# Optimization experiments

Measured on AMD Instinct MI355X. Metric: run time of the kernel, lower is better.

## Reference

```python
import jax, jax.numpy as jnp
import numpy as np

NUM_HEADS = 4
GROUPS = 8
EPS = 1e-5


def group_norm(x, w, b):
    B, C, H, W = x.shape
    xg = x.reshape(B, GROUPS, C // GROUPS, H, W)
    mu = jnp.mean(xg, axis=(2, 3, 4), keepdims=True)
    var = jnp.var(xg, axis=(2, 3, 4), keepdims=True)
    xg = (xg - mu) * jax.lax.rsqrt(var + EPS)
    x = xg.reshape(B, C, H, W)
    return x * w[None, :, None, None] + b[None, :, None, None]


def setup_inputs() -> dict:
    key = jax.random.key(0)
    k1, k2, k3 = jax.random.split(key, 3)
    B, C, H, W = 16, 256, 32, 32
    x = jax.random.normal(k1, (B, C, H, W), dtype=jnp.float32)
    gn_w = jnp.ones((C,), dtype=jnp.float32)
    gn_b = jnp.zeros((C,), dtype=jnp.float32)
    qkv_w = jax.random.normal(k2, (3 * C, C), dtype=jnp.float32) * 0.02
    qkv_b = jnp.zeros((3 * C,), dtype=jnp.float32)
    proj_w = jax.random.normal(k3, (C, C), dtype=jnp.float32) * 0.02
    proj_b = jnp.zeros((C,), dtype=jnp.float32)
    return {"x": x, "gn_w": gn_w, "gn_b": gn_b, "qkv_w": qkv_w,
            "qkv_b": qkv_b, "proj_w": proj_w, "proj_b": proj_b}


def reference(x, gn_w, gn_b, qkv_w, qkv_b, proj_w, proj_b):
    B, C, H, W = x.shape
    Dh = C // NUM_HEADS
    N = H * W
    skip = x
    xn = group_norm(x, gn_w, gn_b)
    # 1x1 conv QKV projection: [B,3C,H,W]
    qkv = jnp.einsum('oc,bchw->bohw', qkv_w, xn) + qkv_b[None, :, None, None]
    # split channel dim 3C -> [3, heads, Dh], flatten spatial -> N
    qkv = qkv.reshape(B, 3, NUM_HEADS, Dh, N)
    qkv = jnp.transpose(qkv, (1, 0, 2, 4, 3))  # [3,B,heads,N,Dh]
    q, k, v = qkv[0], qkv[1], qkv[2]
    scale = 1.0 / np.sqrt(Dh).astype(np.float32)
    attn = jnp.einsum('bhnd,bhmd->bhnm', q, k) * scale  # [B,heads,N,N]
    attn = jax.nn.softmax(attn, axis=-1)
    out = jnp.einsum('bhnm,bhmd->bhnd', attn, v)  # [B,heads,N,Dh]
    out = jnp.transpose(out, (0, 1, 3, 2)).reshape(B, C, H, W)
    out = jnp.einsum('oc,bchw->bohw', proj_w, out) + proj_b[None, :, None, None]
    return out + skip
```

## Files before the change

### kernel.cpp

```cpp
#include <hip/hip_runtime.h>

typedef unsigned short u16;
typedef __bf16 bf16x8 __attribute__((ext_vector_type(8)));
typedef float f32x4 __attribute__((ext_vector_type(4)));

#define QSCALE 0.18033688011112042f

__device__ __forceinline__ u16 f2bf(float f) {
  __bf16 h = (__bf16)f;
  union { __bf16 b; u16 u; } cv;
  cv.b = h;
  return cv.u;
}
__device__ __forceinline__ unsigned pack2(float a, float b) {
  return (unsigned)f2bf(a) | ((unsigned)f2bf(b) << 16);
}

__global__ __launch_bounds__(256) void prep(
    const float* __restrict__ qw, const float* __restrict__ pw,
    const float* __restrict__ x,
    u16* __restrict__ qwb, u16* __restrict__ pwb, float* __restrict__ stats) {
  __shared__ float sh1[256], sh2[256];
  const int blk = blockIdx.x;
  const int t = threadIdx.x;
  if (blk < 256) {
    int i = blk * 256 + t;
    const float* s; u16* d; int j;
    if (i < 49152) { s = qw; d = qwb; j = i; }
    else           { s = pw; d = pwb; j = i - 49152; }
    float4 v = *(const float4*)(s + (size_t)j * 4);
    uint2 o; o.x = pack2(v.x, v.y); o.y = pack2(v.z, v.w);
    *(uint2*)(d + (size_t)j * 4) = o;
    return;
  }
  const int bid = blk - 256;
  int cl = t >> 3;
  int off = (t & 7) * 4;
  const float* p = x + (size_t)bid * 32768 + (size_t)cl * 1024 + off;
  float s = 0.f, ss = 0.f;
#pragma unroll 8
  for (int i = 0; i < 32; ++i) {
    float4 v = *(const float4*)(p + i * 32);
    s += v.x + v.y + v.z + v.w;
    ss += v.x * v.x + v.y * v.y + v.z * v.z + v.w * v.w;
  }
  sh1[t] = s; sh2[t] = ss;
  __syncthreads();
  for (int st = 128; st > 0; st >>= 1) {
    if (t < st) { sh1[t] += sh1[t + st]; sh2[t] += sh2[t + st]; }
    __syncthreads();
  }
  if (t == 0) {
    float mean = sh1[0] * (1.f / 32768.f);
    float var = sh2[0] * (1.f / 32768.f) - mean * mean;
    stats[bid * 2] = mean;
    stats[bid * 2 + 1] = rsqrtf(var + 1e-5f);
  }
}

__global__ __launch_bounds__(256) void gemm_qkv(
    const u16* __restrict__ A, const float* __restrict__ x,
    const float* __restrict__ stats,
    const float* __restrict__ gw, const float* __restrict__ gb,
    const float* __restrict__ bias,
    u16* __restrict__ o_q, u16* __restrict__ o_k, u16* __restrict__ o_v) {
  const int l = blockIdx.x;
  const int xcd = l & 7;
  const int i2 = l >> 3;
  const int m_t = i2 % 6;
  const int nl6 = i2 / 6;
  const int nt = xcd * 16 + nl6;
  const int m0 = m_t * 128;
  const int n0 = nt * 128;
  const int b = nt >> 3;
  const int nsp0 = (nt & 7) * 128;

  const int t = threadIdx.x;
  const int wave = t >> 6, lane = t & 63, lm = lane & 15, quad = lane >> 4;
  const int wr = wave >> 1, wc = wave & 1;

  __shared__ u16 As[2][128 * 32];
  __shared__ u16 Bs[2][128 * 32];

  f32x4 acc[4][4];
  const f32x4 fzero = {0.f, 0.f, 0.f, 0.f};
#pragma unroll
  for (int i = 0; i < 4; ++i)
#pragma unroll
    for (int j = 0; j < 4; ++j) acc[i][j] = fzero;

  const int srow = t >> 2, scol = (t & 3) * 8;
  const u16* pA0 = A + (size_t)(m0 + srow) * 256 + scol;
  const u16* pA1 = A + (size_t)(m0 + 64 + srow) * 256 + scol;

  const int n2 = t & 63, gq = t >> 6;
  const float* xb = x + (size_t)b * 262144 + nsp0 + 2 * n2;
  const int gsw = (gq ^ (n2 & 3)) * 8;
  u16* const bd0 = (u16*)0;
  (void)bd0;

  float2 vB[8];
  uint4 vA0, vA1;

#define LD_B(ki)                                                       \
  {                                                                    \
    const int cb = (ki) * 32 + gq * 8;                                 \
    _Pragma("unroll") for (int i = 0; i < 8; ++i)                      \
        vB[i] = *(const float2*)(xb + (size_t)(cb + i) * 1024);        \
  }
#define ST_B(ki, buf)                                                  \
  {                                                                    \
    const int cb = (ki) * 32 + gq * 8;                                 \
    const float mu = stats[(b * 8 + (ki)) * 2];                        \
    const float rq = stats[(b * 8 + (ki)) * 2 + 1];                    \
    float e0[8], e1[8];                                                \
    _Pragma("unroll") for (int i = 0; i < 8; ++i) {                    \
      const float w = gw[cb + i] * rq;                                 \
      const float bb = gb[cb + i] - mu * w;                            \
      e0[i] = vB[i].x * w + bb;                                        \
      e1[i] = vB[i].y * w + bb;                                        \
    }                                                                  \
    uint4 w0, w1;                                                      \
    w0.x = pack2(e0[0], e0[1]); w0.y = pack2(e0[2], e0[3]);            \
    w0.z = pack2(e0[4], e0[5]); w0.w = pack2(e0[6], e0[7]);            \
    w1.x = pack2(e1[0], e1[1]); w1.y = pack2(e1[2], e1[3]);            \
    w1.z = pack2(e1[4], e1[5]); w1.w = pack2(e1[6], e1[7]);            \
    *(uint4*)(Bs[buf] + (2 * n2) * 32 + gsw) = w0;                     \
    *(uint4*)(Bs[buf] + (2 * n2 + 1) * 32 + gsw) = w1;                 \
  }

  LD_B(0);
  vA0 = *(const uint4*)pA0;
  vA1 = *(const uint4*)pA1;
  ST_B(0, 0);
  *(uint4*)(As[0] + srow * 32 + scol) = vA0;
  *(uint4*)(As[0] + (64 + srow) * 32 + scol) = vA1;
  LD_B(1);
  vA0 = *(const uint4*)(pA0 + 32);
  vA1 = *(const uint4*)(pA1 + 32);

  for (int ki = 0; ki < 8; ++ki) {
    __syncthreads();
    if (ki + 1 < 8) {
      ST_B(ki + 1, (ki + 1) & 1);
      u16* as = As[(ki + 1) & 1];
      *(uint4*)(as + srow * 32 + scol) = vA0;
      *(uint4*)(as + (64 + srow) * 32 + scol) = vA1;
    }
    if (ki + 2 < 8) {
      LD_B(ki + 2);
      vA0 = *(const uint4*)(pA0 + (ki + 2) * 32);
      vA1 = *(const uint4*)(pA1 + (ki + 2) * 32);
    }
    if (ki + 1 < 8) __syncthreads();
    const u16* as = As[ki & 1];
    const u16* bs = Bs[ki & 1];
    bf16x8 af[4], bf[4];
#pragma unroll
    for (int mb = 0; mb < 4; ++mb)
      af[mb] = *(const bf16x8*)(as + (wr * 64 + mb * 16 + lm) * 32 + quad * 8);
#pragma unroll
    for (int nb = 0; nb < 4; ++nb) {
      const int row = wc * 64 + nb * 16 + lm;
      bf[nb] = *(const bf16x8*)(bs + row * 32 + ((quad ^ ((row >> 1) & 3)) * 8));
    }
#pragma unroll
    for (int mb = 0; mb < 4; ++mb)
#pragma unroll
      for (int nb = 0; nb < 4; ++nb)
        acc[mb][nb] = __builtin_amdgcn_mfma_f32_16x16x32_bf16(af[mb], bf[nb],
                                                              acc[mb][nb], 0, 0, 0);
  }
#undef LD_B
#undef ST_B

#pragma unroll
  for (int mb = 0; mb < 4; ++mb) {
#pragma unroll
    for (int nb = 0; nb < 4; ++nb) {
      const int o = m0 + wr * 64 + mb * 16 + 4 * quad;
      const int ng = n0 + wc * 64 + nb * 16 + lm;
      const int bb = ng >> 10, n = ng & 1023;
      const int kind = o >> 8;
      if (kind == 1) {
        ushort4 pk;
        pk.x = f2bf(acc[mb][nb][0] + bias[o]);
        pk.y = f2bf(acc[mb][nb][1] + bias[o + 1]);
        pk.z = f2bf(acc[mb][nb][2] + bias[o + 2]);
        pk.w = f2bf(acc[mb][nb][3] + bias[o + 3]);
        const int h = (o >> 6) & 3;
        *(ushort4*)(o_k + ((size_t)((bb * 4 + h) * 1024 + n)) * 64 + (o & 63)) = pk;
      } else {
        u16* dst = (kind == 0) ? o_q : o_v;
        const float sc = (kind == 0) ? QSCALE : 1.f;
        const int oc = o & 255;
#pragma unroll
        for (int r = 0; r < 4; ++r)
          dst[((size_t)(bb * 256 + oc + r)) * 1024 + n] =
              f2bf((acc[mb][nb][r] + bias[o + r]) * sc);
      }
    }
  }
}

__global__ __launch_bounds__(256) void gemm_proj(
    const u16* __restrict__ A, const u16* __restrict__ Bm,
    const float* __restrict__ bias,
    const float* __restrict__ skip, float* __restrict__ out) {
  const int m0 = blockIdx.y * 64;
  const int n0 = blockIdx.x * 128;
  const int t = threadIdx.x;
  const int wave = t >> 6, lane = t & 63, lm = lane & 15, quad = lane >> 4;
  const int wr = wave >> 1, wc = wave & 1;

  __shared__ u16 As[2][64 * 32];
  __shared__ u16 Bs[2][128 * 32];

  f32x4 acc[2][4];
  const f32x4 fzero = {0.f, 0.f, 0.f, 0.f};
#pragma unroll
  for (int i = 0; i < 2; ++i)
#pragma unroll
    for (int j = 0; j < 4; ++j) acc[i][j] = fzero;

  const int srow = t >> 2, scol = (t & 3) * 8;
  const u16* pA0 = A + (size_t)(m0 + srow) * 256 + scol;
  const u16* pB0 = Bm + (size_t)(n0 + srow) * 256 + scol;
  const u16* pB1 = Bm + (size_t)(n0 + 64 + srow) * 256 + scol;

  uint4 pa0 = *(const uint4*)pA0;
  uint4 pb0 = *(const uint4*)pB0;
  uint4 pb1 = *(const uint4*)pB1;
  *(uint4*)(As[0] + srow * 32 + scol) = pa0;
  *(uint4*)(Bs[0] + srow * 32 + scol) = pb0;
  *(uint4*)(Bs[0] + (64 + srow) * 32 + scol) = pb1;
  pa0 = *(const uint4*)(pA0 + 32);
  pb0 = *(const uint4*)(pB0 + 32);
  pb1 = *(const uint4*)(pB1 + 32);

  for (int ki = 0; ki < 8; ++ki) {
    __syncthreads();
    if (ki + 1 < 8) {
      u16* as = As[(ki + 1) & 1];
      u16* bs = Bs[(ki + 1) & 1];
      *(uint4*)(as + srow * 32 + scol) = pa0;
      *(uint4*)(bs + srow * 32 + scol) = pb0;
      *(uint4*)(bs + (64 + srow) * 32 + scol) = pb1;
    }
    if (ki + 2 < 8) {
      const int ko = (ki + 2) * 32;
      pa0 = *(const uint4*)(pA0 + ko);
      pb0 = *(const uint4*)(pB0 + ko);
      pb1 = *(const uint4*)(pB1 + ko);
    }
    if (ki + 1 < 8) __syncthreads();
    const u16* as = As[ki & 1];
    const u16* bs = Bs[ki & 1];
    bf16x8 af[2], bf[4];
#pragma unroll
    for (int mb = 0; mb < 2; ++mb)
      af[mb] = *(const bf16x8*)(as + (wr * 32 + mb * 16 + lm) * 32 + quad * 8);
#pragma unroll
    for (int nb = 0; nb < 4; ++nb)
      bf[nb] = *(const bf16x8*)(bs + (wc * 64 + nb * 16 + lm) * 32 + quad * 8);
#pragma unroll
    for (int mb = 0; mb < 2; ++mb)
#pragma unroll
      for (int nb = 0; nb < 4; ++nb)
        acc[mb][nb] = __builtin_amdgcn_mfma_f32_16x16x32_bf16(af[mb], bf[nb],
                                                              acc[mb][nb], 0, 0, 0);
  }

#pragma unroll
  for (int mb = 0; mb < 2; ++mb) {
#pragma unroll
    for (int nb = 0; nb < 4; ++nb) {
      const int o = m0 + wr * 32 + mb * 16 + 4 * quad;
      const int ng = n0 + wc * 64 + nb * 16 + lm;
      const int b = ng >> 10, n = ng & 1023;
#pragma unroll
      for (int r = 0; r < 4; ++r) {
        const size_t oi = ((size_t)(b * 256 + o + r)) * 1024 + n;
        out[oi] = acc[mb][nb][r] + bias[o + r] + skip[oi];
      }
    }
  }
}

__global__ __launch_bounds__(256) void attn_fused(
    const u16* __restrict__ qdn, const u16* __restrict__ knd,
    const u16* __restrict__ vdn, u16* __restrict__ att) {
  const int bid = blockIdx.x;
  const int bh = (bid & 7) * 8 + ((bid >> 3) & 7);
  const int qtile = bid >> 6;
  const int t = threadIdx.x;
  const int wave = t >> 6, lane = t & 63, lm = lane & 15, quad = lane >> 4;

  const u16* qb = qdn + (size_t)bh * 65536;
  const u16* kb = knd + (size_t)bh * 65536;
  const u16* vb = vdn + (size_t)bh * 65536;

  __shared__ u16 KV[2][2][64 * 64];
  __shared__ u16 QP[64 * 64];

  const int e1 = t + 256;
  const int r0 = t >> 3, c0_ = t & 7, r1 = e1 >> 3, c1_ = e1 & 7;
  const int lk0 = r0 * 64 + ((c0_ ^ (r0 & 7)) * 8);
  const int lk1 = r1 * 64 + ((c1_ ^ (r1 & 7)) * 8);
  const u16* kg0 = kb + r0 * 64 + c0_ * 8;
  const u16* kg1 = kb + r1 * 64 + c1_ * 8;
  const u16* vg0 = vb + r0 * 1024 + c0_ * 8;
  const u16* vg1 = vb + r1 * 1024 + c1_ * 8;

  uint4 pk0 = *(const uint4*)kg0;
  uint4 pk1 = *(const uint4*)kg1;
  uint4 pv0 = *(const uint4*)vg0;
  uint4 pv1 = *(const uint4*)vg1;

  {
    union { uint4 v; u16 s[8]; } tq0, tq1;
    const int d0 = t >> 3, ngq = t & 7;
    tq0.v = *(const uint4*)(qb + (size_t)d0 * 1024 + qtile * 64 + ngq * 8);
    tq1.v = *(const uint4*)(qb + (size_t)(32 + d0) * 1024 + qtile * 64 + ngq * 8);
    const int oa = d0 >> 3, ob = 4 + oa, dl = d0 & 7;
#pragma unroll
    for (int k = 0; k < 8; ++k) {
      const int row = ngq * 8 + k;
      QP[row * 64 + ((oa ^ k) * 8) + dl] = tq0.s[k];
      QP[row * 64 + ((ob ^ k) * 8) + dl] = tq1.s[k];
    }
  }

  *(uint4*)(KV[0][0] + lk0) = pk0;
  *(uint4*)(KV[0][0] + lk1) = pk1;
  *(uint4*)(KV[0][1] + lk0) = pv0;
  *(uint4*)(KV[0][1] + lk1) = pv1;
  pk0 = *(const uint4*)(kg0 + 4096);
  pk1 = *(const uint4*)(kg1 + 4096);
  pv0 = *(const uint4*)(vg0 + 64);
  pv1 = *(const uint4*)(vg1 + 64);
  __syncthreads();

  const int swz0 = (quad ^ (lm & 7)) * 8;
  const int swz1 = ((4 + quad) ^ (lm & 7)) * 8;
  u16* Pw = QP + (wave * 16 + lm) * 64;
  const bf16x8 qf0 = *(const bf16x8*)(Pw + swz0);
  const bf16x8 qf1 = *(const bf16x8*)(Pw + swz1);

  const f32x4 fzero = {0.f, 0.f, 0.f, 0.f};
  f32x4 oacc[4];
#pragma unroll
  for (int d = 0; d < 4; ++d) oacc[d] = fzero;
  float lp = 0.f;

  for (int jc = 0; jc < 16; ++jc) {
    if (jc) __syncthreads();
    if (jc + 1 < 16) {
      u16* kd = KV[(jc + 1) & 1][0];
      u16* vd = KV[(jc + 1) & 1][1];
      *(uint4*)(kd + lk0) = pk0;
      *(uint4*)(kd + lk1) = pk1;
      *(uint4*)(vd + lk0) = pv0;
      *(uint4*)(vd + lk1) = pv1;
    }
    if (jc + 2 < 16) {
      pk0 = *(const uint4*)(kg0 + (jc + 2) * 4096);
      pk1 = *(const uint4*)(kg1 + (jc + 2) * 4096);
      pv0 = *(const uint4*)(vg0 + (jc + 2) * 64);
      pv1 = *(const uint4*)(vg1 + (jc + 2) * 64);
    }
    const u16* Ks = KV[jc & 1][0];
    const u16* Vs = KV[jc & 1][1];

    f32x4 sacc[4];
#pragma unroll
    for (int jb = 0; jb < 4; ++jb) sacc[jb] = fzero;
#pragma unroll
    for (int jb = 0; jb < 4; ++jb) {
      const int row = (jb * 16 + lm) * 64;
      bf16x8 kf0 = *(const bf16x8*)(Ks + row + swz0);
      bf16x8 kf1 = *(const bf16x8*)(Ks + row + swz1);
      sacc[jb] = __builtin_amdgcn_mfma_f32_16x16x32_bf16(kf0, qf0, sacc[jb], 0, 0, 0);
      sacc[jb] = __builtin_amdgcn_mfma_f32_16x16x32_bf16(kf1, qf1, sacc[jb], 0, 0, 0);
    }
#pragma unroll
    for (int jb = 0; jb < 4; ++jb) {
      const float e0 = exp2f(sacc[jb][0]);
      const float ee1 = exp2f(sacc[jb][1]);
      const float e2 = exp2f(sacc[jb][2]);
      const float e3 = exp2f(sacc[jb][3]);
      lp += (e0 + ee1) + (e2 + e3);
      uint2 pw;
      pw.x = pack2(e0, ee1);
      pw.y = pack2(e2, e3);
      const int oct = 2 * jb + (quad >> 1);
      *(uint2*)(Pw + ((oct ^ (lm & 7)) * 8) + 4 * (quad & 1)) = pw;
    }
    bf16x8 pf0 = *(const bf16x8*)(Pw + swz0);
    bf16x8 pf1 = *(const bf16x8*)(Pw + swz1);
#pragma unroll
    for (int db = 0; db < 4; ++db) {
      const int row = (db * 16 + lm) * 64;
      bf16x8 vf0 = *(const bf16x8*)(Vs + row + swz0);
      bf16x8 vf1 = *(const bf16x8*)(Vs + row + swz1);
      oacc[db] = __builtin_amdgcn_mfma_f32_16x16x32_bf16(pf0, vf0, oacc[db], 0, 0, 0);
      oacc[db] = __builtin_amdgcn_mfma_f32_16x16x32_bf16(pf1, vf1, oacc[db], 0, 0, 0);
    }
  }

  float rs = lp;
  rs += __shfl_xor(rs, 16);
  rs += __shfl_xor(rs, 32);
  const int b = bh >> 2, h = bh & 3;
#pragma unroll
  for (int r = 0; r < 4; ++r) {
    const float inv = 1.f / __shfl(rs, 4 * quad + r);
    const int n = qtile * 64 + wave * 16 + 4 * quad + r;
#pragma unroll
    for (int db = 0; db < 4; ++db) {
      const int c = h * 64 + db * 16 + lm;
      att[((size_t)(b * 1024 + n)) * 256 + c] = f2bf(oacc[db][r] * inv);
    }
  }
}

extern "C" void kernel_launch(void* const* d_in, const int* in_sizes, int n_in,
                              void* d_out, int out_size, void* d_ws, size_t ws_size,
                              hipStream_t stream) {
  const float* x      = (const float*)d_in[0];
  const float* gn_w   = (const float*)d_in[1];
  const float* gn_b   = (const float*)d_in[2];
  const float* qkv_w  = (const float*)d_in[3];
  const float* qkv_b  = (const float*)d_in[4];
  const float* proj_w = (const float*)d_in[5];
  const float* proj_b = (const float*)d_in[6];
  float* out = (float*)d_out;

  char* ws = (char*)d_ws;
  float* stats = (float*)(ws + 0);
  u16* qwb = (u16*)(ws + 4096);
  u16* pwb = (u16*)(ws + 397312);
  u16* qdn = (u16*)(ws + 8916992);
  u16* knd = (u16*)(ws + 17305600);
  u16* vdn = (u16*)(ws + 25694208);
  u16* att = (u16*)(ws + 34082816);

  prep<<<384, 256, 0, stream>>>(qkv_w, proj_w, x, qwb, pwb, stats);
  gemm_qkv<<<768, 256, 0, stream>>>(qwb, x, stats, gn_w, gn_b, qkv_b,
                                    qdn, knd, vdn);
  attn_fused<<<1024, 256, 0, stream>>>(qdn, knd, vdn, att);
  gemm_proj<<<dim3(128, 4), 256, 0, stream>>>(pwb, att, proj_b, x, out);
}
```

Measured before the change: 142.9 us.

## Give each attention wave two query tiles and drop redundant GEMM barriers

The attention kernel now runs with 128 threads per block, and each wave handles 32 query rows instead of 16. Every K and V fragment loaded from LDS therefore feeds two MFMA chains, which halves the LDS fragment traffic per query. The K/V staging loops are widened to match, exp2f is replaced with the hardware exp2 builtin, and bf16 packing uses the packed convert instruction when it is available. The second __syncthreads inside both GEMM double-buffer loops is removed, since the barrier at the top of the next iteration already orders those stores. In exchange the attention kernel has fewer waves per block and higher register pressure, which may lower latency hiding.

Result: slower. 185.8 us (+30.1%).

```diff
diff --git a/kernel.cpp b/kernel.cpp
--- a/kernel.cpp
+++ b/kernel.cpp
@@ -13,7 +13,18 @@
   return cv.u;
 }
 __device__ __forceinline__ unsigned pack2(float a, float b) {
+#if __has_builtin(__builtin_amdgcn_cvt_pk_bf16_f32)
+  typedef __bf16 bf16x2 __attribute__((ext_vector_type(2)));
+  bf16x2 p = __builtin_amdgcn_cvt_pk_bf16_f32(a, b);
+  union { bf16x2 v; unsigned u; } cv;
+  cv.v = p;
+  return cv.u;
+#else
   return (unsigned)f2bf(a) | ((unsigned)f2bf(b) << 16);
+#endif
+}
+__device__ __forceinline__ float fexp2(float x) {
+  return __builtin_amdgcn_exp2f(x);
 }
 
 __global__ __launch_bounds__(256) void prep(
@@ -96,8 +107,6 @@
   const int n2 = t & 63, gq = t >> 6;
   const float* xb = x + (size_t)b * 262144 + nsp0 + 2 * n2;
   const int gsw = (gq ^ (n2 & 3)) * 8;
-  u16* const bd0 = (u16*)0;
-  (void)bd0;
 
   float2 vB[8];
   uint4 vA0, vA1;
@@ -152,7 +161,6 @@
       vA0 = *(const uint4*)(pA0 + (ki + 2) * 32);
       vA1 = *(const uint4*)(pA1 + (ki + 2) * 32);
     }
-    if (ki + 1 < 8) __syncthreads();
     const u16* as = As[ki & 1];
     const u16* bs = Bs[ki & 1];
     bf16x8 af[4], bf[4];
@@ -253,7 +261,6 @@
       pb0 = *(const uint4*)(pB0 + ko);
       pb1 = *(const uint4*)(pB1 + ko);
     }
-    if (ki + 1 < 8) __syncthreads();
     const u16* as = As[ki & 1];
     const u16* bs = Bs[ki & 1];
     bf16x8 af[2], bf[4];
@@ -287,7 +294,7 @@
   }
 }
 
-__global__ __launch_bounds__(256) void attn_fused(
+__global__ __launch_bounds__(128) void attn_fused(
     const u16* __restrict__ qdn, const u16* __restrict__ knd,
     const u16* __restrict__ vdn, u16* __restrict__ att) {
   const int bid = blockIdx.x;
@@ -303,123 +310,157 @@
   __shared__ u16 KV[2][2][64 * 64];
   __shared__ u16 QP[64 * 64];
 
-  const int e1 = t + 256;
-  const int r0 = t >> 3, c0_ = t & 7, r1 = e1 >> 3, c1_ = e1 & 7;
-  const int lk0 = r0 * 64 + ((c0_ ^ (r0 & 7)) * 8);
-  const int lk1 = r1 * 64 + ((c1_ ^ (r1 & 7)) * 8);
-  const u16* kg0 = kb + r0 * 64 + c0_ * 8;
-  const u16* kg1 = kb + r1 * 64 + c1_ * 8;
-  const u16* vg0 = vb + r0 * 1024 + c0_ * 8;
-  const u16* vg1 = vb + r1 * 1024 + c1_ * 8;
-
-  uint4 pk0 = *(const uint4*)kg0;
-  uint4 pk1 = *(const uint4*)kg1;
-  uint4 pv0 = *(const uint4*)vg0;
-  uint4 pv1 = *(const uint4*)vg1;
+  int lk_[4];
+  const u16 *kg_[4], *vg_[4];
+#pragma unroll
+  for (int i = 0; i < 4; ++i) {
+    const int e = t + 128 * i;
+    const int r = e >> 3, c = e & 7;
+    lk_[i] = r * 64 + ((c ^ (r & 7)) * 8);
+    kg_[i] = kb + r * 64 + c * 8;
+    vg_[i] = vb + r * 1024 + c * 8;
+  }
+  uint4 pk[4], pv[4];
+#pragma unroll
+  for (int i = 0; i < 4; ++i) {
+    pk[i] = *(const uint4*)kg_[i];
+    pv[i] = *(const uint4*)vg_[i];
+  }
 
   {
-    union { uint4 v; u16 s[8]; } tq0, tq1;
-    const int d0 = t >> 3, ngq = t & 7;
-    tq0.v = *(const uint4*)(qb + (size_t)d0 * 1024 + qtile * 64 + ngq * 8);
-    tq1.v = *(const uint4*)(qb + (size_t)(32 + d0) * 1024 + qtile * 64 + ngq * 8);
-    const int oa = d0 >> 3, ob = 4 + oa, dl = d0 & 7;
-#pragma unroll
-    for (int k = 0; k < 8; ++k) {
-      const int row = ngq * 8 + k;
-      QP[row * 64 + ((oa ^ k) * 8) + dl] = tq0.s[k];
-      QP[row * 64 + ((ob ^ k) * 8) + dl] = tq1.s[k];
-    }
-  }
-
-  *(uint4*)(KV[0][0] + lk0) = pk0;
-  *(uint4*)(KV[0][0] + lk1) = pk1;
-  *(uint4*)(KV[0][1] + lk0) = pv0;
-  *(uint4*)(KV[0][1] + lk1) = pv1;
-  pk0 = *(const uint4*)(kg0 + 4096);
-  pk1 = *(const uint4*)(kg1 + 4096);
-  pv0 = *(const uint4*)(vg0 + 64);
-  pv1 = *(const uint4*)(vg1 + 64);
+    const int dbase = t >> 3, ngq = t & 7;
+#pragma unroll
+    for (int s = 0; s < 4; ++s) {
+      const int d0 = dbase + 16 * s;
+      union { uint4 v; u16 sv[8]; } tq;
+      tq.v = *(const uint4*)(qb + (size_t)d0 * 1024 + qtile * 64 + ngq * 8);
+      const int oa = d0 >> 3, dl = d0 & 7;
+#pragma unroll
+      for (int k = 0; k < 8; ++k) {
+        const int row = ngq * 8 + k;
+        QP[row * 64 + ((oa ^ k) * 8) + dl] = tq.sv[k];
+      }
+    }
+  }
+
+#pragma unroll
+  for (int i = 0; i < 4; ++i) {
+    *(uint4*)(KV[0][0] + lk_[i]) = pk[i];
+    *(uint4*)(KV[0][1] + lk_[i]) = pv[i];
+  }
+#pragma unroll
+  for (int i = 0; i < 4; ++i) {
+    pk[i] = *(const uint4*)(kg_[i] + 4096);
+    pv[i] = *(const uint4*)(vg_[i] + 64);
+  }
   __syncthreads();
 
   const int swz0 = (quad ^ (lm & 7)) * 8;
   const int swz1 = ((4 + quad) ^ (lm & 7)) * 8;
-  u16* Pw = QP + (wave * 16 + lm) * 64;
-  const bf16x8 qf0 = *(const bf16x8*)(Pw + swz0);
-  const bf16x8 qf1 = *(const bf16x8*)(Pw + swz1);
+
+  bf16x8 qf[2][2];
+  u16* Prow[2];
+#pragma unroll
+  for (int ib = 0; ib < 2; ++ib) {
+    u16* rp = QP + (wave * 32 + ib * 16 + lm) * 64;
+    qf[ib][0] = *(const bf16x8*)(rp + swz0);
+    qf[ib][1] = *(const bf16x8*)(rp + swz1);
+    Prow[ib] = rp;
+  }
 
   const f32x4 fzero = {0.f, 0.f, 0.f, 0.f};
-  f32x4 oacc[4];
-#pragma unroll
-  for (int d = 0; d < 4; ++d) oacc[d] = fzero;
-  float lp = 0.f;
+  f32x4 oacc[2][4];
+#pragma unroll
+  for (int ib = 0; ib < 2; ++ib)
+#pragma unroll
+    for (int d = 0; d < 4; ++d) oacc[ib][d] = fzero;
+  float lp[2] = {0.f, 0.f};
 
   for (int jc = 0; jc < 16; ++jc) {
     if (jc) __syncthreads();
     if (jc + 1 < 16) {
       u16* kd = KV[(jc + 1) & 1][0];
       u16* vd = KV[(jc + 1) & 1][1];
-      *(uint4*)(kd + lk0) = pk0;
-      *(uint4*)(kd + lk1) = pk1;
-      *(uint4*)(vd + lk0) = pv0;
-      *(uint4*)(vd + lk1) = pv1;
+#pragma unroll
+      for (int i = 0; i < 4; ++i) {
+        *(uint4*)(kd + lk_[i]) = pk[i];
+        *(uint4*)(vd + lk_[i]) = pv[i];
+      }
     }
     if (jc + 2 < 16) {
-      pk0 = *(const uint4*)(kg0 + (jc + 2) * 4096);
-      pk1 = *(const uint4*)(kg1 + (jc + 2) * 4096);
-      pv0 = *(const uint4*)(vg0 + (jc + 2) * 64);
-      pv1 = *(const uint4*)(vg1 + (jc + 2) * 64);
+#pragma unroll
+      for (int i = 0; i < 4; ++i) {
+        pk[i] = *(const uint4*)(kg_[i] + (jc + 2) * 4096);
+        pv[i] = *(const uint4*)(vg_[i] + (jc + 2) * 64);
+      }
     }
     const u16* Ks = KV[jc & 1][0];
     const u16* Vs = KV[jc & 1][1];
 
-    f32x4 sacc[4];
-#pragma unroll
-    for (int jb = 0; jb < 4; ++jb) sacc[jb] = fzero;
+    f32x4 sacc[2][4];
+#pragma unroll
+    for (int ib = 0; ib < 2; ++ib)
+#pragma unroll
+      for (int jb = 0; jb < 4; ++jb) sacc[ib][jb] = fzero;
 #pragma unroll
     for (int jb = 0; jb < 4; ++jb) {
       const int row = (jb * 16 + lm) * 64;
       bf16x8 kf0 = *(const bf16x8*)(Ks + row + swz0);
       bf16x8 kf1 = *(const bf16x8*)(Ks + row + swz1);
-      sacc[jb] = __builtin_amdgcn_mfma_f32_16x16x32_bf16(kf0, qf0, sacc[jb], 0, 0, 0);
-      sacc[jb] = __builtin_amdgcn_mfma_f32_16x16x32_bf16(kf1, qf1, sacc[jb], 0, 0, 0);
-    }
-#pragma unroll
-    for (int jb = 0; jb < 4; ++jb) {
-      const float e0 = exp2f(sacc[jb][0]);
-      const float ee1 = exp2f(sacc[jb][1]);
-      const float e2 = exp2f(sacc[jb][2]);
-      const float e3 = exp2f(sacc[jb][3]);
-      lp += (e0 + ee1) + (e2 + e3);
-      uint2 pw;
-      pw.x = pack2(e0, ee1);
-      pw.y = pack2(e2, e3);
-      const int oct = 2 * jb + (quad >> 1);
-      *(uint2*)(Pw + ((oct ^ (lm & 7)) * 8) + 4 * (quad & 1)) = pw;
-    }
-    bf16x8 pf0 = *(const bf16x8*)(Pw + swz0);
-    bf16x8 pf1 = *(const bf16x8*)(Pw + swz1);
+      sacc[0][jb] = __builtin_amdgcn_mfma_f32_16x16x32_bf16(kf0, qf[0][0], sacc[0][jb], 0, 0, 0);
+      sacc[0][jb] = __builtin_amdgcn_mfma_f32_16x16x32_bf16(kf1, qf[0][1], sacc[0][jb], 0, 0, 0);
+      sacc[1][jb] = __builtin_amdgcn_mfma_f32_16x16x32_bf16(kf0, qf[1][0], sacc[1][jb], 0, 0, 0);
+      sacc[1][jb] = __builtin_amdgcn_mfma_f32_16x16x32_bf16(kf1, qf[1][1], sacc[1][jb], 0, 0, 0);
+    }
+#pragma unroll
+    for (int ib = 0; ib < 2; ++ib) {
+#pragma unroll
+      for (int jb = 0; jb < 4; ++jb) {
+        const float e0 = fexp2(sacc[ib][jb][0]);
+        const float e1 = fexp2(sacc[ib][jb][1]);
+        const float e2 = fexp2(sacc[ib][jb][2]);
+        const float e3 = fexp2(sacc[ib][jb][3]);
+        lp[ib] += (e0 + e1) + (e2 + e3);
+        uint2 pw;
+        pw.x = pack2(e0, e1);
+        pw.y = pack2(e2, e3);
+        const int oct = 2 * jb + (quad >> 1);
+        *(uint2*)(Prow[ib] + ((oct ^ (lm & 7)) * 8) + 4 * (quad & 1)) = pw;
+      }
+    }
+    bf16x8 pf[2][2];
+#pragma unroll
+    for (int ib = 0; ib < 2; ++ib) {
+      pf[ib][0] = *(const bf16x8*)(Prow[ib] + swz0);
+      pf[ib][1] = *(const bf16x8*)(Prow[ib] + swz1);
+    }
 #pragma unroll
     for (int db = 0; db < 4; ++db) {
       const int row = (db * 16 + lm) * 64;
       bf16x8 vf0 = *(const bf16x8*)(Vs + row + swz0);
       bf16x8 vf1 = *(const bf16x8*)(Vs + row + swz1);
-      oacc[db] = __builtin_amdgcn_mfma_f32_16x16x32_bf16(pf0, vf0, oacc[db], 0, 0, 0);
-      oacc[db] = __builtin_amdgcn_mfma_f32_16x16x32_bf16(pf1, vf1, oacc[db], 0, 0, 0);
-    }
-  }
-
-  float rs = lp;
-  rs += __shfl_xor(rs, 16);
-  rs += __shfl_xor(rs, 32);
+      oacc[0][db] = __builtin_amdgcn_mfma_f32_16x16x32_bf16(pf[0][0], vf0, oacc[0][db], 0, 0, 0);
+      oacc[0][db] = __builtin_amdgcn_mfma_f32_16x16x32_bf16(pf[0][1], vf1, oacc[0][db], 0, 0, 0);
+      oacc[1][db] = __builtin_amdgcn_mfma_f32_16x16x32_bf16(pf[1][0], vf0, oacc[1][db], 0, 0, 0);
+      oacc[1][db] = __builtin_amdgcn_mfma_f32_16x16x32_bf16(pf[1][1], vf1, oacc[1][db], 0, 0, 0);
+    }
+  }
+
   const int b = bh >> 2, h = bh & 3;
 #pragma unroll
-  for (int r = 0; r < 4; ++r) {
-    const float inv = 1.f / __shfl(rs, 4 * quad + r);
-    const int n = qtile * 64 + wave * 16 + 4 * quad + r;
-#pragma unroll
-    for (int db = 0; db < 4; ++db) {
-      const int c = h * 64 + db * 16 + lm;
-      att[((size_t)(b * 1024 + n)) * 256 + c] = f2bf(oacc[db][r] * inv);
+  for (int ib = 0; ib < 2; ++ib) {
+    float rs = lp[ib];
+    rs += __shfl_xor(rs, 16);
+    rs += __shfl_xor(rs, 32);
+#pragma unroll
+    for (int r = 0; r < 4; ++r) {
+      const float inv = 1.f / __shfl(rs, 4 * quad + r);
+      const int n = qtile * 64 + wave * 32 + ib * 16 + 4 * quad + r;
+#pragma unroll
+      for (int db = 0; db < 4; ++db) {
+        const int c = h * 64 + db * 16 + lm;
+        att[((size_t)(b * 1024 + n)) * 256 + c] = f2bf(oacc[ib][db][r] * inv);
+      }
     }
   }
 }
@@ -448,6 +489,6 @@
   prep<<<384, 256, 0, stream>>>(qkv_w, proj_w, x, qwb, pwb, stats);
   gemm_qkv<<<768, 256, 0, stream>>>(qwb, x, stats, gn_w, gn_b, qkv_b,
                                     qdn, knd, vdn);
-  attn_fused<<<1024, 256, 0, stream>>>(qdn, knd, vdn, att);
+  attn_fused<<<1024, 128, 0, stream>>>(qdn, knd, vdn, att);
   gemm_proj<<<dim3(128, 4), 256, 0, stream>>>(pwb, att, proj_b, x, out);
 }
```
